# Optimization experiments

Hardware: AMD Instinct MI355X
Metric: run time of the kernel (lower is better)

The kernel has to match this reference:

```python
import jax, jax.numpy as jnp
import numpy as np
from jax import lax

H = 128

def lstm_layer(x, w_ih, w_hh, b):
    # x: [T,B,I]; w_ih: [4H,I]; w_hh: [4H,H]; b: [4H] (b_ih+b_hh combined)
    T, B, _ = x.shape
    Hs = w_hh.shape[1]
    xg = jnp.einsum('tbi,gi->tbg', x, w_ih) + b  # precompute input projections [T,B,4H]
    def step(carry, xg_t):
        h, c = carry
        g = xg_t + h @ w_hh.T
        i, f, gg, o = jnp.split(g, 4, axis=-1)  # PyTorch gate order: i,f,g,o
        c = jax.nn.sigmoid(f) * c + jax.nn.sigmoid(i) * jnp.tanh(gg)
        h = jax.nn.sigmoid(o) * jnp.tanh(c)
        return (h, c), h
    init = (jnp.zeros((B, Hs), x.dtype), jnp.zeros((B, Hs), x.dtype))
    (h_n, c_n), hs = lax.scan(step, init, xg)
    return hs, (h_n, c_n)

def setup_inputs() -> dict:
    key = jax.random.key(0)
    ks = jax.random.split(key, 12)
    V, T, B = 32000, 512, 64
    s = 1.0 / np.sqrt(H)
    u = lambda k, sh: jax.random.uniform(k, sh, jnp.float32, -s, s)
    return {
        'inputs': jax.random.randint(ks[0], (T, B), 0, V),
        'emb': jax.random.normal(ks[1], (V, H), jnp.float32),
        'w_ih0': u(ks[2], (2, 4 * H, H)),      # bidirectional layer 0 (fwd, bwd)
        'w_hh0': u(ks[3], (2, 4 * H, H)),
        'b0':    u(ks[4], (2, 4 * H)),
        'w_ih1': u(ks[5], (4 * H, 2 * H)),     # layer 1 consumes concat of both directions
        'w_hh1': u(ks[6], (4 * H, H)),
        'b1':    u(ks[7], (4 * H)),
        'w_ihr': u(ks[8], (6, 4 * H, H)),      # layers 2..7 (residual)
        'w_hhr': u(ks[9], (6, 4 * H, H)),
        'br':    u(ks[10], (6, 4 * H)),
    }

def reference(inputs, emb, w_ih0, w_hh0, b0, w_ih1, w_hh1, b1, w_ihr, w_hhr, br):
    x = emb[inputs]                                   # [T,B,H]
    # layer 0: bidirectional
    hf, _ = lstm_layer(x, w_ih0[0], w_hh0[0], b0[0])
    hb, _ = lstm_layer(x[::-1], w_ih0[1], w_hh0[1], b0[1])
    x = jnp.concatenate([hf, hb[::-1]], axis=-1)      # [T,B,2H]
    # layer 1: 2H -> H
    x, hidden = lstm_layer(x, w_ih1, w_hh1, b1)
    # layers 2..7 with residual adds
    for i in range(w_ihr.shape[0]):
        residual = x
        x, hidden = lstm_layer(x, w_ihr[i], w_hhr[i], br[i])
        x = x + residual
    h_n, c_n = hidden
    return x, h_n[None], c_n[None]
```

## Files before the change

kernel.cpp:

```cpp
#include <hip/hip_runtime.h>
#include <hip/hip_bf16.h>

#define TT 512
#define BB 64
#define HH 128
#define GG 512
#define TBH (TT*BB*HH)
#define TBG (TT*BB*GG)
#define BH (BB*HH)
#define CH 64
#define NCH (TT/CH)
#define CHGG (CH*BB*GG)
#define CHH (CH*BB*HH)

__device__ __forceinline__ float bflo(unsigned u) { return __uint_as_float(u << 16); }
__device__ __forceinline__ float bfhi(unsigned u) { return __uint_as_float(u & 0xffff0000u); }
__device__ __forceinline__ float ldf(const void* p, size_t i, int isbf) {
  return isbf ? __uint_as_float(((unsigned)((const unsigned short*)p)[i]) << 16)
              : ((const float*)p)[i];
}

template<int CTRL>
__device__ __forceinline__ float dpp_add(float v) {
  int r = __builtin_amdgcn_mov_dpp(__float_as_int(v), CTRL, 0xF, 0xF, true);
  return v + __int_as_float(r);
}

__device__ __forceinline__ float sigm(float x) {
  return __builtin_amdgcn_rcpf(1.f + __expf(-x));
}
__device__ __forceinline__ float tanh_f(float x) {
  return fmaf(2.f, __builtin_amdgcn_rcpf(1.f + __expf(-2.f * x)), -1.f);
}

__device__ __forceinline__ void ldw16(const void* W, size_t off, int isbf, float4* out) {
  if (isbf) {
    const uint4* wp = (const uint4*)W;
    uint4 v0 = wp[(off >> 3) + 0];
    uint4 v1 = wp[(off >> 3) + 1];
    out[0] = make_float4(bflo(v0.x), bfhi(v0.x), bflo(v0.y), bfhi(v0.y));
    out[1] = make_float4(bflo(v0.z), bfhi(v0.z), bflo(v0.w), bfhi(v0.w));
    out[2] = make_float4(bflo(v1.x), bfhi(v1.x), bflo(v1.y), bfhi(v1.y));
    out[3] = make_float4(bflo(v1.z), bfhi(v1.z), bflo(v1.w), bfhi(v1.w));
  } else {
    const float4* wp = (const float4*)W;
    out[0] = wp[(off >> 2) + 0]; out[1] = wp[(off >> 2) + 1];
    out[2] = wp[(off >> 2) + 2]; out[3] = wp[(off >> 2) + 3];
  }
}

__global__ __launch_bounds__(256) void k_detect(const unsigned* __restrict__ bits,
                                                unsigned* __restrict__ flag) {
  __shared__ int cnt;
  if (threadIdx.x == 0) cnt = 0;
  __syncthreads();
  int local = 0;
  for (int i = threadIdx.x; i < 1024; i += 256) {
    unsigned e = (bits[i] >> 7) & 0xff;
    if (e >= 118 && e <= 134) local++;
  }
  atomicAdd(&cnt, local);
  __syncthreads();
  if (threadIdx.x == 0) *flag = (cnt > 768) ? 1u : 0u;
}

__global__ __launch_bounds__(256) void k_embed(const int* __restrict__ idx,
                                               const void* __restrict__ emb,
                                               const unsigned* __restrict__ flag,
                                               float* __restrict__ x0) {
  int isbf = (int)*flag;
  int i = blockIdx.x * 256 + threadIdx.x;
  int h = i & (HH - 1);
  int tb = i >> 7;
  x0[i] = ldf(emb, (size_t)idx[tb] * HH + h, isbf);
}

__global__ __launch_bounds__(256) void k_proj(const float* __restrict__ A,
                                              const void* __restrict__ W, size_t w_off,
                                              const void* __restrict__ bias, size_t b_off,
                                              float* __restrict__ C, int K,
                                              const unsigned* __restrict__ flag) {
  int isbf = (int)*flag;
  __shared__ float As[16][68];
  __shared__ float Bs[16][68];
  int tid = threadIdx.x;
  int tx = tid & 15, ty = tid >> 4;
  int m_base = blockIdx.x * 64, n_base = blockIdx.y * 64;
  float acc[4][4] = {};
  int kk = tid & 15, rr = tid >> 4;
  for (int k0 = 0; k0 < K; k0 += 16) {
    #pragma unroll
    for (int r = 0; r < 4; r++) {
      As[kk][rr + 16*r] = A[(size_t)(m_base + rr + 16*r) * K + k0 + kk];
      Bs[kk][rr + 16*r] = ldf(W, w_off + (size_t)(n_base + rr + 16*r) * K + k0 + kk, isbf);
    }
    __syncthreads();
    #pragma unroll
    for (int k = 0; k < 16; k++) {
      float4 av = *(const float4*)(&As[k][ty*4]);
      float4 bv = *(const float4*)(&Bs[k][tx*4]);
      float a[4] = {av.x, av.y, av.z, av.w};
      float b[4] = {bv.x, bv.y, bv.z, bv.w};
      #pragma unroll
      for (int i = 0; i < 4; i++)
        #pragma unroll
        for (int j = 0; j < 4; j++)
          acc[i][j] += a[i] * b[j];
    }
    __syncthreads();
  }
  #pragma unroll
  for (int i = 0; i < 4; i++) {
    #pragma unroll
    for (int j = 0; j < 4; j++) {
      int n = n_base + tx*4 + j;
      C[(size_t)(m_base + ty*4 + i) * GG + n] = acc[i][j] + ldf(bias, b_off + n, isbf);
    }
  }
}

__global__ __launch_bounds__(512, 2) void k_recur(
    const float* __restrict__ xg, size_t xg_dstride,
    const void* __restrict__ whh, size_t w_off, size_t w_dstride,
    float* __restrict__ hout, int hout_stride, int hout_doff,
    const float* __restrict__ res,
    float* __restrict__ hfin, float* __restrict__ cfin,
    int bidir, const unsigned* __restrict__ flag) {
  int isbf = (int)*flag;
  int d = blockIdx.x >> 6;
  int b = blockIdx.x & 63;
  int dir = (bidir == 2 || (bidir == 1 && d)) ? -1 : 1;
  xg += (size_t)d * xg_dstride;
  size_t woff = w_off + (size_t)d * w_dstride;
  int hcol = hout_doff * d;

  int t0 = threadIdx.x;
  int j = t0 >> 2, q = t0 & 3;

  float w[4][32];
  size_t wbase = woff + (size_t)j * HH + q * 32;
  if (isbf) {
    const uint4* wp = (const uint4*)whh;
    #pragma unroll
    for (int g = 0; g < 4; g++) {
      size_t b8 = (wbase + (size_t)g * 128 * HH) >> 3;
      #pragma unroll
      for (int u = 0; u < 4; u++) {
        uint4 v = wp[b8 + ((u + q) & 3)];
        w[g][u*8+0] = bflo(v.x); w[g][u*8+1] = bfhi(v.x);
        w[g][u*8+2] = bflo(v.y); w[g][u*8+3] = bfhi(v.y);
        w[g][u*8+4] = bflo(v.z); w[g][u*8+5] = bfhi(v.z);
        w[g][u*8+6] = bflo(v.w); w[g][u*8+7] = bfhi(v.w);
      }
    }
  } else {
    const float4* wp = (const float4*)whh;
    #pragma unroll
    for (int g = 0; g < 4; g++) {
      size_t b4 = (wbase + (size_t)g * 128 * HH) >> 2;
      #pragma unroll
      for (int u = 0; u < 8; u++) {
        float4 v = wp[b4 + ((u + 2*q) & 7)];
        w[g][u*4+0] = v.x; w[g][u*4+1] = v.y; w[g][u*4+2] = v.z; w[g][u*4+3] = v.w;
      }
    }
  }

  __shared__ float h_lds[2][HH];
  if (t0 < HH) h_lds[0][t0] = 0.f;
  float c = 0.f;

  int tfirst = (dir > 0) ? 0 : (TT - 1);
  size_t rg0 = ((size_t)tfirst * BB + b) * GG;
  float xg_cur[4];
  #pragma unroll
  for (int g = 0; g < 4; g++) xg_cur[g] = xg[rg0 + g * HH + j];
  float res_cur = res ? res[((size_t)tfirst * BB + b) * HH + j] : 0.f;
  __syncthreads();

  const float* hc = h_lds[0];
  float* hn = h_lds[1];

  #pragma unroll 1
  for (int s = 0; s < TT; s++) {
    int t = (dir > 0) ? s : (TT - 1 - s);
    float xg_nxt[4] = {0.f, 0.f, 0.f, 0.f};
    float res_nxt = 0.f;
    if (s + 1 < TT) {
      int tn = (dir > 0) ? (s + 1) : (TT - 2 - s);
      size_t rg = ((size_t)tn * BB + b) * GG;
      #pragma unroll
      for (int g = 0; g < 4; g++) xg_nxt[g] = xg[rg + g * HH + j];
      if (res) res_nxt = res[((size_t)tn * BB + b) * HH + j];
    }
    float p0 = 0.f, p1 = 0.f, p2 = 0.f, p3 = 0.f;
    const float4* hq = (const float4*)(hc + (q << 5));
    #pragma unroll
    for (int u = 0; u < 8; u++) {
      float4 hv = hq[(u + 2*q) & 7];
      p0 = fmaf(w[0][u*4+0], hv.x, p0); p0 = fmaf(w[0][u*4+1], hv.y, p0);
      p0 = fmaf(w[0][u*4+2], hv.z, p0); p0 = fmaf(w[0][u*4+3], hv.w, p0);
      p1 = fmaf(w[1][u*4+0], hv.x, p1); p1 = fmaf(w[1][u*4+1], hv.y, p1);
      p1 = fmaf(w[1][u*4+2], hv.z, p1); p1 = fmaf(w[1][u*4+3], hv.w, p1);
      p2 = fmaf(w[2][u*4+0], hv.x, p2); p2 = fmaf(w[2][u*4+1], hv.y, p2);
      p2 = fmaf(w[2][u*4+2], hv.z, p2); p2 = fmaf(w[2][u*4+3], hv.w, p2);
      p3 = fmaf(w[3][u*4+0], hv.x, p3); p3 = fmaf(w[3][u*4+1], hv.y, p3);
      p3 = fmaf(w[3][u*4+2], hv.z, p3); p3 = fmaf(w[3][u*4+3], hv.w, p3);
    }
    p0 = dpp_add<0xB1>(p0); p0 = dpp_add<0x4E>(p0);
    p1 = dpp_add<0xB1>(p1); p1 = dpp_add<0x4E>(p1);
    p2 = dpp_add<0xB1>(p2); p2 = dpp_add<0x4E>(p2);
    p3 = dpp_add<0xB1>(p3); p3 = dpp_add<0x4E>(p3);

    float gi = p0 + xg_cur[0], gf = p1 + xg_cur[1];
    float gc = p2 + xg_cur[2], go = p3 + xg_cur[3];
    float si = sigm(gi), sf = sigm(gf), so = sigm(go);
    c = fmaf(sf, c, si * tanh_f(gc));
    float h = so * tanh_f(c);

    if (q == 0) {
      hn[j] = h;
      hout[((size_t)t * BB + b) * hout_stride + hcol + j] = h + res_cur;
      if (t == TT - 1) hfin[(size_t)(d * BB + b) * HH + j] = h;
    }
    #pragma unroll
    for (int g = 0; g < 4; g++) xg_cur[g] = xg_nxt[g];
    res_cur = res_nxt;
    __syncthreads();
    const float* tmp = hc; hc = hn; hn = (float*)tmp;
  }
  if (q == 0) cfin[(size_t)(d * BB + b) * HH + j] = c;
}

struct WaveDesc { int n; int r[8]; int k[8]; };

__device__ __forceinline__ void colgemm4(
    const float (*hch)[264], int K,
    const void* W, size_t wbase,
    const void* bias, size_t bias_off, int isbf,
    float* dstbase, int nn, int mh) {
  float acc[4][16];
  #pragma unroll
  for (int c = 0; c < 4; c++) {
    float bv = ldf(bias, bias_off + nn + 128*c, isbf);
    #pragma unroll
    for (int mi = 0; mi < 16; mi++) acc[c][mi] = bv;
  }
  #pragma unroll 1
  for (int kb = 0; kb < K; kb += 16) {
    float4 wcb[4][4];
    #pragma unroll
    for (int c = 0; c < 4; c++)
      ldw16(W, wbase + (size_t)(nn + 128*c) * K + kb, isbf, wcb[c]);
    #pragma unroll
    for (int mi = 0; mi < 16; mi++) {
      const float* hrow = &hch[mh*16 + mi][kb];
      float4 hv[4];
      hv[0] = *(const float4*)&hrow[0];
      hv[1] = *(const float4*)&hrow[4];
      hv[2] = *(const float4*)&hrow[8];
      hv[3] = *(const float4*)&hrow[12];
      #pragma unroll
      for (int c = 0; c < 4; c++) {
        #pragma unroll
        for (int u = 0; u < 4; u++) {
          acc[c][mi] = fmaf(wcb[c][u].x, hv[u].x, acc[c][mi]);
          acc[c][mi] = fmaf(wcb[c][u].y, hv[u].y, acc[c][mi]);
          acc[c][mi] = fmaf(wcb[c][u].z, hv[u].z, acc[c][mi]);
          acc[c][mi] = fmaf(wcb[c][u].w, hv[u].w, acc[c][mi]);
        }
      }
    }
  }
  #pragma unroll
  for (int mi = 0; mi < 16; mi++) {
    size_t mo = (size_t)(mh*16 + mi) * BB * GG;
    #pragma unroll
    for (int c = 0; c < 4; c++)
      dstbase[mo + nn + 128*c] = acc[c][mi];
  }
}

__global__ __launch_bounds__(512, 1) void k_wave(
    WaveDesc wd, float* __restrict__ xgf, float* __restrict__ xgb,
    const float* __restrict__ xcat, float* __restrict__ out7, float* __restrict__ scratch,
    const void* __restrict__ w_ih1, const void* __restrict__ w_hh1, const void* __restrict__ b1,
    const void* __restrict__ w_ihr, const void* __restrict__ w_hhr, const void* __restrict__ br,
    const unsigned* __restrict__ flag) {
  int isbf = (int)*flag;
  int slot = blockIdx.x >> 6;
  int b = blockIdx.x & 63;
  int r = wd.r[slot];
  int k = wd.k[slot];

  float* ringbase = xgb + 4 * (size_t)CHGG;
  float* hstate   = ringbase + 12 * (size_t)CHH;
  float* cstate   = hstate + 7 * (size_t)BH;

  auto xgslot = [&](int rr, int kk) -> float* {
    int s = (rr - 2) * 2 + (kk & 1);
    return (s < 8) ? (xgf + (size_t)s * CHGG) : (xgb + (size_t)(s - 8) * CHGG);
  };
  auto ringch = [&](int rr, int kk) -> float* {
    return ringbase + ((size_t)(rr - 1) * 2 + (kk & 1)) * CHH;
  };

  __shared__ float hchunk[CH][264];
  __shared__ float h_lds[2][HH];

  int t0 = threadIdx.x;
  int nn = t0 & 127;
  int mh = t0 >> 7;

  if (r == 1) {
    {
      int m = t0 >> 3, c0 = (t0 & 7) * 32;
      const float* src = xcat + ((size_t)(k * CH + m) * BB + b) * (2 * HH) + c0;
      #pragma unroll
      for (int u = 0; u < 8; u++)
        *(float4*)&hchunk[m][c0 + u * 4] = ((const float4*)src)[u];
    }
    __syncthreads();
    colgemm4(hchunk, 2 * HH, w_ih1, 0, b1, 0, isbf,
             scratch + (size_t)b * GG, nn, mh);
    __syncthreads();
  }

  const void* whh = (r == 1) ? w_hh1 : w_hhr;
  size_t woff = (r == 1) ? 0 : (size_t)(r - 2) * GG * HH;
  const float* xg = (r == 1) ? scratch : xgslot(r, k);
  const float* resb = (r >= 2) ? (ringch(r - 1, k) + (size_t)b * HH) : nullptr;
  float* houtb = (r == 7) ? (out7 + (size_t)k * CHH + (size_t)b * HH)
                          : (ringch(r, k) + (size_t)b * HH);
  float* hst = hstate + (size_t)(r - 1) * BH + (size_t)b * HH;
  float* cst = cstate + (size_t)(r - 1) * BH + (size_t)b * HH;

  int j = t0 >> 2, q = t0 & 3;

  float w[4][32];
  size_t wbase = woff + (size_t)j * HH + q * 32;
  if (isbf) {
    const uint4* wp = (const uint4*)whh;
    #pragma unroll
    for (int g = 0; g < 4; g++) {
      size_t b8 = (wbase + (size_t)g * 128 * HH) >> 3;
      #pragma unroll
      for (int u = 0; u < 4; u++) {
        uint4 v = wp[b8 + ((u + q) & 3)];
        w[g][u*8+0] = bflo(v.x); w[g][u*8+1] = bfhi(v.x);
        w[g][u*8+2] = bflo(v.y); w[g][u*8+3] = bfhi(v.y);
        w[g][u*8+4] = bflo(v.z); w[g][u*8+5] = bfhi(v.z);
        w[g][u*8+6] = bflo(v.w); w[g][u*8+7] = bfhi(v.w);
      }
    }
  } else {
    const float4* wp = (const float4*)whh;
    #pragma unroll
    for (int g = 0; g < 4; g++) {
      size_t b4 = (wbase + (size_t)g * 128 * HH) >> 2;
      #pragma unroll
      for (int u = 0; u < 8; u++) {
        float4 v = wp[b4 + ((u + 2*q) & 7)];
        w[g][u*4+0] = v.x; w[g][u*4+1] = v.y; w[g][u*4+2] = v.z; w[g][u*4+3] = v.w;
      }
    }
  }

  if (t0 < HH) h_lds[0][t0] = k ? hst[t0] : 0.f;
  float c = k ? cst[j] : 0.f;

  size_t rg0 = (size_t)b * GG;
  float xg_cur[4];
  #pragma unroll
  for (int g = 0; g < 4; g++) xg_cur[g] = xg[rg0 + g * HH + j];
  float res_cur = resb ? resb[j] : 0.f;
  __syncthreads();

  const float* hc = h_lds[0];
  float* hn = h_lds[1];

  #pragma unroll 1
  for (int s = 0; s < CH; s++) {
    float xg_nxt[4] = {0.f, 0.f, 0.f, 0.f};
    float res_nxt = 0.f;
    if (s + 1 < CH) {
      size_t rg = ((size_t)(s + 1) * BB + b) * GG;
      #pragma unroll
      for (int g = 0; g < 4; g++) xg_nxt[g] = xg[rg + g * HH + j];
      if (resb) res_nxt = resb[(size_t)(s + 1) * BB * HH + j];
    }
    float p0 = 0.f, p1 = 0.f, p2 = 0.f, p3 = 0.f;
    const float4* hq = (const float4*)(hc + (q << 5));
    #pragma unroll
    for (int u = 0; u < 8; u++) {
      float4 hv = hq[(u + 2*q) & 7];
      p0 = fmaf(w[0][u*4+0], hv.x, p0); p0 = fmaf(w[0][u*4+1], hv.y, p0);
      p0 = fmaf(w[0][u*4+2], hv.z, p0); p0 = fmaf(w[0][u*4+3], hv.w, p0);
      p1 = fmaf(w[1][u*4+0], hv.x, p1); p1 = fmaf(w[1][u*4+1], hv.y, p1);
      p1 = fmaf(w[1][u*4+2], hv.z, p1); p1 = fmaf(w[1][u*4+3], hv.w, p1);
      p2 = fmaf(w[2][u*4+0], hv.x, p2); p2 = fmaf(w[2][u*4+1], hv.y, p2);
      p2 = fmaf(w[2][u*4+2], hv.z, p2); p2 = fmaf(w[2][u*4+3], hv.w, p2);
      p3 = fmaf(w[3][u*4+0], hv.x, p3); p3 = fmaf(w[3][u*4+1], hv.y, p3);
      p3 = fmaf(w[3][u*4+2], hv.z, p3); p3 = fmaf(w[3][u*4+3], hv.w, p3);
    }
    p0 = dpp_add<0xB1>(p0); p0 = dpp_add<0x4E>(p0);
    p1 = dpp_add<0xB1>(p1); p1 = dpp_add<0x4E>(p1);
    p2 = dpp_add<0xB1>(p2); p2 = dpp_add<0x4E>(p2);
    p3 = dpp_add<0xB1>(p3); p3 = dpp_add<0x4E>(p3);

    float gi = p0 + xg_cur[0], gf = p1 + xg_cur[1];
    float gc = p2 + xg_cur[2], go = p3 + xg_cur[3];
    float si = sigm(gi), sf = sigm(gf), so = sigm(go);
    c = fmaf(sf, c, si * tanh_f(gc));
    float h = so * tanh_f(c);

    if (q == 0) {
      float hv = h + res_cur;
      hn[j] = h;
      hchunk[s][j] = hv;
      houtb[(size_t)s * BB * HH + j] = hv;
      if (s == CH - 1) hst[j] = h;
    }
    #pragma unroll
    for (int g = 0; g < 4; g++) xg_cur[g] = xg_nxt[g];
    res_cur = res_nxt;
    __syncthreads();
    const float* tmp = hc; hc = hn; hn = (float*)tmp;
  }
  if (q == 0) cst[j] = c;

  if (r < 7) {
    colgemm4(hchunk, HH, w_ihr, (size_t)(r - 1) * GG * HH,
             br, (size_t)(r - 1) * GG, isbf,
             xgslot(r + 1, k) + (size_t)b * GG, nn, mh);
  }
}

__global__ __launch_bounds__(256) void k_out(const float* __restrict__ x,
                                             const float* __restrict__ hfin,
                                             const float* __restrict__ cfin,
                                             void* __restrict__ out,
                                             const unsigned* __restrict__ flag) {
  int isbf = (int)*flag;
  int i = blockIdx.x * 256 + threadIdx.x;
  float v;
  if (i < TBH) v = x[i];
  else if (i < TBH + BH) v = hfin[i - TBH];
  else v = cfin[i - TBH - BH];
  if (isbf) ((__hip_bfloat16*)out)[i] = __float2bfloat16(v);
  else ((float*)out)[i] = v;
}

extern "C" void kernel_launch(void* const* d_in, const int* in_sizes, int n_in,
                              void* d_out, int out_size, void* d_ws, size_t ws_size,
                              hipStream_t stream) {
  const int* idx = (const int*)d_in[0];
  const void* emb   = d_in[1];
  const void* w_ih0 = d_in[2];
  const void* w_hh0 = d_in[3];
  const void* b0    = d_in[4];
  const void* w_ih1 = d_in[5];
  const void* w_hh1 = d_in[6];
  const void* b1    = d_in[7];
  const void* w_ihr = d_in[8];
  const void* w_hhr = d_in[9];
  const void* br    = d_in[10];

  float* ws   = (float*)d_ws;
  float* x0   = ws;
  float* xcat = ws + TBH;
  float* xg_f = ws + 3 * (size_t)TBH;
  float* hfin = ws + 3 * (size_t)TBH + TBG;
  float* cfin = hfin + 2 * BH;
  unsigned* flag = (unsigned*)(cfin + 2 * BH);
  float* xg_b = cfin + 2 * BH + 16384;
  int merged = ws_size >= (size_t)(3 * (size_t)TBH + 2 * (size_t)TBG + 4 * BH + 16384 + 64) * 4;

  k_detect<<<1, 256, 0, stream>>>((const unsigned*)emb, flag);
  k_embed<<<TBH / 256, 256, 0, stream>>>(idx, emb, flag, x0);

  dim3 pg(512, 8);
  if (merged) {
    k_proj<<<pg, 256, 0, stream>>>(x0, w_ih0, 0, b0, 0, xg_f, HH, flag);
    k_proj<<<pg, 256, 0, stream>>>(x0, w_ih0, (size_t)GG * HH, b0, GG, xg_b, HH, flag);
    k_recur<<<128, 512, 0, stream>>>(xg_f, (size_t)(xg_b - xg_f), w_hh0, 0, (size_t)GG * HH,
                                     xcat, 2 * HH, HH, nullptr, hfin, cfin, 1, flag);

    float* scratch = x0 + (size_t)TBH / 2;
    float* ringbase = xg_b + 4 * (size_t)CHGG;
    float* hstate  = ringbase + 12 * (size_t)CHH;
    float* cstate  = hstate + 7 * (size_t)BH;
    for (int wv = 0; wv <= 6 + (NCH - 1); wv++) {
      WaveDesc wd; wd.n = 0;
      for (int r = 1; r <= 7; r++) {
        int kk = wv - (r - 1);
        if (kk >= 0 && kk < NCH) { wd.r[wd.n] = r; wd.k[wd.n] = kk; wd.n++; }
      }
      if (wd.n)
        k_wave<<<wd.n * 64, 512, 0, stream>>>(wd, xg_f, xg_b, xcat, x0, scratch,
                                              w_ih1, w_hh1, b1, w_ihr, w_hhr, br, flag);
    }
    k_out<<<(TBH + 2 * BH) / 256, 256, 0, stream>>>(x0, hstate + 6 * BH, cstate + 6 * BH,
                                                    d_out, flag);
  } else {
    k_proj<<<pg, 256, 0, stream>>>(x0, w_ih0, 0, b0, 0, xg_f, HH, flag);
    k_recur<<<64, 512, 0, stream>>>(xg_f, 0, w_hh0, 0, 0,
                                    xcat, 2 * HH, 0, nullptr, hfin, cfin, 0, flag);
    k_proj<<<pg, 256, 0, stream>>>(x0, w_ih0, (size_t)GG * HH, b0, GG, xg_f, HH, flag);
    k_recur<<<64, 512, 0, stream>>>(xg_f, 0, w_hh0, (size_t)GG * HH, 0,
                                    xcat + HH, 2 * HH, 0, nullptr, hfin, cfin, 2, flag);
    float* xA = xcat;
    float* xB = xcat + TBH;
    k_proj<<<pg, 256, 0, stream>>>(xcat, w_ih1, 0, b1, 0, xg_f, 2 * HH, flag);
    k_recur<<<64, 512, 0, stream>>>(xg_f, 0, w_hh1, 0, 0, xA, HH, 0, nullptr, hfin, cfin, 0, flag);
    float* cur = xA;
    float* nxt = xB;
    for (int r = 0; r < 6; r++) {
      k_proj<<<pg, 256, 0, stream>>>(cur, w_ihr, (size_t)r * GG * HH, br, (size_t)r * GG, xg_f, HH, flag);
      k_recur<<<64, 512, 0, stream>>>(xg_f, 0, w_hhr, (size_t)r * GG * HH, 0,
                                      nxt, HH, 0, cur, hfin, cfin, 0, flag);
      float* t = cur; cur = nxt; nxt = t;
    }
    k_out<<<(TBH + 2 * BH) / 256, 256, 0, stream>>>(cur, hfin, cfin, d_out, flag);
  }
}
```

Before: 2.642 ms.

## Process two batch rows per block in wavefront LSTM kernel

Each k_wave block now runs the recurrence for two batch rows at once, so the grid shrinks from 64 to 32 blocks per wave slot. The register-held recurrent weights are reused across both rows, and the barrier and reduction costs of each time step are shared between them. In exchange each step does twice the serial FMA and transcendental work per thread with half as many blocks in flight. The chunk staging buffer in LDS is split into two 132-stride halves, one per row, and the input-projection GEMMs are run per row.

```diff
diff --git a/kernel.cpp b/kernel.cpp
--- a/kernel.cpp
+++ b/kernel.cpp
@@ -235,7 +235,7 @@
 struct WaveDesc { int n; int r[8]; int k[8]; };
 
 __device__ __forceinline__ void colgemm4(
-    const float (*hch)[264], int K,
+    const float* hch, int rstride, int K,
     const void* W, size_t wbase,
     const void* bias, size_t bias_off, int isbf,
     float* dstbase, int nn, int mh) {
@@ -254,7 +254,7 @@
       ldw16(W, wbase + (size_t)(nn + 128*c) * K + kb, isbf, wcb[c]);
     #pragma unroll
     for (int mi = 0; mi < 16; mi++) {
-      const float* hrow = &hch[mh*16 + mi][kb];
+      const float* hrow = hch + (size_t)(mh*16 + mi) * rstride + kb;
       float4 hv[4];
       hv[0] = *(const float4*)&hrow[0];
       hv[1] = *(const float4*)&hrow[4];
@@ -288,8 +288,9 @@
     const void* __restrict__ w_ihr, const void* __restrict__ w_hhr, const void* __restrict__ br,
     const unsigned* __restrict__ flag) {
   int isbf = (int)*flag;
-  int slot = blockIdx.x >> 6;
-  int b = blockIdx.x & 63;
+  int slot = blockIdx.x >> 5;
+  int bb = blockIdx.x & 31;
+  int bA = bb * 2, bB = bb * 2 + 1;
   int r = wd.r[slot];
   int k = wd.k[slot];
 
@@ -305,35 +306,44 @@
     return ringbase + ((size_t)(rr - 1) * 2 + (kk & 1)) * CHH;
   };
 
-  __shared__ float hchunk[CH][264];
-  __shared__ float h_lds[2][HH];
+  __shared__ float pool[CH * 264];
+  __shared__ float hldsA[2][HH];
+  __shared__ float hldsB[2][HH];
+  float* stg = pool;
+  float* pA  = pool;
+  float* pB  = pool + CH * 132;
 
   int t0 = threadIdx.x;
   int nn = t0 & 127;
   int mh = t0 >> 7;
 
   if (r == 1) {
-    {
-      int m = t0 >> 3, c0 = (t0 & 7) * 32;
-      const float* src = xcat + ((size_t)(k * CH + m) * BB + b) * (2 * HH) + c0;
-      #pragma unroll
-      for (int u = 0; u < 8; u++)
-        *(float4*)&hchunk[m][c0 + u * 4] = ((const float4*)src)[u];
-    }
-    __syncthreads();
-    colgemm4(hchunk, 2 * HH, w_ih1, 0, b1, 0, isbf,
-             scratch + (size_t)b * GG, nn, mh);
-    __syncthreads();
+    #pragma unroll 1
+    for (int pb = 0; pb < 2; pb++) {
+      int b = bA + pb;
+      {
+        int m = t0 >> 3, c0 = (t0 & 7) * 32;
+        const float* src = xcat + ((size_t)(k * CH + m) * BB + b) * (2 * HH) + c0;
+        #pragma unroll
+        for (int u = 0; u < 8; u++)
+          *(float4*)&stg[m * 264 + c0 + u * 4] = ((const float4*)src)[u];
+      }
+      __syncthreads();
+      colgemm4(stg, 264, 2 * HH, w_ih1, 0, b1, 0, isbf,
+               scratch + (size_t)b * GG, nn, mh);
+      __syncthreads();
+    }
   }
 
   const void* whh = (r == 1) ? w_hh1 : w_hhr;
   size_t woff = (r == 1) ? 0 : (size_t)(r - 2) * GG * HH;
   const float* xg = (r == 1) ? scratch : xgslot(r, k);
-  const float* resb = (r >= 2) ? (ringch(r - 1, k) + (size_t)b * HH) : nullptr;
-  float* houtb = (r == 7) ? (out7 + (size_t)k * CHH + (size_t)b * HH)
-                          : (ringch(r, k) + (size_t)b * HH);
-  float* hst = hstate + (size_t)(r - 1) * BH + (size_t)b * HH;
-  float* cst = cstate + (size_t)(r - 1) * BH + (size_t)b * HH;
+  const float* ringp = (r >= 2) ? ringch(r - 1, k) : nullptr;
+  float* houtbase = (r == 7) ? (out7 + (size_t)k * CHH) : ringch(r, k);
+  float* hstA = hstate + (size_t)(r - 1) * BH + (size_t)bA * HH;
+  float* hstB = hstate + (size_t)(r - 1) * BH + (size_t)bB * HH;
+  float* cstA = cstate + (size_t)(r - 1) * BH + (size_t)bA * HH;
+  float* cstB = cstate + (size_t)(r - 1) * BH + (size_t)bB * HH;
 
   int j = t0 >> 2, q = t0 & 3;
 
@@ -366,73 +376,114 @@
     }
   }
 
-  if (t0 < HH) h_lds[0][t0] = k ? hst[t0] : 0.f;
-  float c = k ? cst[j] : 0.f;
-
-  size_t rg0 = (size_t)b * GG;
-  float xg_cur[4];
+  if (t0 < HH) {
+    hldsA[0][t0] = k ? hstA[t0] : 0.f;
+    hldsB[0][t0] = k ? hstB[t0] : 0.f;
+  }
+  float cA = k ? cstA[j] : 0.f;
+  float cB = k ? cstB[j] : 0.f;
+
+  float xgA[4], xgB[4];
   #pragma unroll
-  for (int g = 0; g < 4; g++) xg_cur[g] = xg[rg0 + g * HH + j];
-  float res_cur = resb ? resb[j] : 0.f;
+  for (int g = 0; g < 4; g++) {
+    xgA[g] = xg[(size_t)bA * GG + g * HH + j];
+    xgB[g] = xg[(size_t)bB * GG + g * HH + j];
+  }
+  float resA = ringp ? ringp[(size_t)bA * HH + j] : 0.f;
+  float resB = ringp ? ringp[(size_t)bB * HH + j] : 0.f;
   __syncthreads();
 
-  const float* hc = h_lds[0];
-  float* hn = h_lds[1];
+  const float* hcA = hldsA[0];
+  const float* hcB = hldsB[0];
+  float* hnA = hldsA[1];
+  float* hnB = hldsB[1];
 
   #pragma unroll 1
   for (int s = 0; s < CH; s++) {
-    float xg_nxt[4] = {0.f, 0.f, 0.f, 0.f};
-    float res_nxt = 0.f;
+    float xgA_n[4] = {0.f,0.f,0.f,0.f}, xgB_n[4] = {0.f,0.f,0.f,0.f};
+    float resA_n = 0.f, resB_n = 0.f;
     if (s + 1 < CH) {
-      size_t rg = ((size_t)(s + 1) * BB + b) * GG;
-      #pragma unroll
-      for (int g = 0; g < 4; g++) xg_nxt[g] = xg[rg + g * HH + j];
-      if (resb) res_nxt = resb[(size_t)(s + 1) * BB * HH + j];
-    }
-    float p0 = 0.f, p1 = 0.f, p2 = 0.f, p3 = 0.f;
-    const float4* hq = (const float4*)(hc + (q << 5));
+      size_t rgA = ((size_t)(s + 1) * BB + bA) * GG;
+      #pragma unroll
+      for (int g = 0; g < 4; g++) {
+        xgA_n[g] = xg[rgA + g * HH + j];
+        xgB_n[g] = xg[rgA + GG + g * HH + j];
+      }
+      if (ringp) {
+        resA_n = ringp[((size_t)(s + 1) * BB + bA) * HH + j];
+        resB_n = ringp[((size_t)(s + 1) * BB + bB) * HH + j];
+      }
+    }
+    float pA0 = 0.f, pA1 = 0.f, pA2 = 0.f, pA3 = 0.f;
+    float pB0 = 0.f, pB1 = 0.f, pB2 = 0.f, pB3 = 0.f;
+    const float4* hqA = (const float4*)(hcA + (q << 5));
+    const float4* hqB = (const float4*)(hcB + (q << 5));
     #pragma unroll
     for (int u = 0; u < 8; u++) {
-      float4 hv = hq[(u + 2*q) & 7];
-      p0 = fmaf(w[0][u*4+0], hv.x, p0); p0 = fmaf(w[0][u*4+1], hv.y, p0);
-      p0 = fmaf(w[0][u*4+2], hv.z, p0); p0 = fmaf(w[0][u*4+3], hv.w, p0);
-      p1 = fmaf(w[1][u*4+0], hv.x, p1); p1 = fmaf(w[1][u*4+1], hv.y, p1);
-      p1 = fmaf(w[1][u*4+2], hv.z, p1); p1 = fmaf(w[1][u*4+3], hv.w, p1);
-      p2 = fmaf(w[2][u*4+0], hv.x, p2); p2 = fmaf(w[2][u*4+1], hv.y, p2);
-      p2 = fmaf(w[2][u*4+2], hv.z, p2); p2 = fmaf(w[2][u*4+3], hv.w, p2);
-      p3 = fmaf(w[3][u*4+0], hv.x, p3); p3 = fmaf(w[3][u*4+1], hv.y, p3);
-      p3 = fmaf(w[3][u*4+2], hv.z, p3); p3 = fmaf(w[3][u*4+3], hv.w, p3);
-    }
-    p0 = dpp_add<0xB1>(p0); p0 = dpp_add<0x4E>(p0);
-    p1 = dpp_add<0xB1>(p1); p1 = dpp_add<0x4E>(p1);
-    p2 = dpp_add<0xB1>(p2); p2 = dpp_add<0x4E>(p2);
-    p3 = dpp_add<0xB1>(p3); p3 = dpp_add<0x4E>(p3);
-
-    float gi = p0 + xg_cur[0], gf = p1 + xg_cur[1];
-    float gc = p2 + xg_cur[2], go = p3 + xg_cur[3];
-    float si = sigm(gi), sf = sigm(gf), so = sigm(go);
-    c = fmaf(sf, c, si * tanh_f(gc));
-    float h = so * tanh_f(c);
+      float4 a = hqA[(u + 2*q) & 7];
+      float4 e = hqB[(u + 2*q) & 7];
+      pA0 = fmaf(w[0][u*4+0], a.x, pA0); pA0 = fmaf(w[0][u*4+1], a.y, pA0);
+      pA0 = fmaf(w[0][u*4+2], a.z, pA0); pA0 = fmaf(w[0][u*4+3], a.w, pA0);
+      pA1 = fmaf(w[1][u*4+0], a.x, pA1); pA1 = fmaf(w[1][u*4+1], a.y, pA1);
+      pA1 = fmaf(w[1][u*4+2], a.z, pA1); pA1 = fmaf(w[1][u*4+3], a.w, pA1);
+      pA2 = fmaf(w[2][u*4+0], a.x, pA2); pA2 = fmaf(w[2][u*4+1], a.y, pA2);
+      pA2 = fmaf(w[2][u*4+2], a.z, pA2); pA2 = fmaf(w[2][u*4+3], a.w, pA2);
+      pA3 = fmaf(w[3][u*4+0], a.x, pA3); pA3 = fmaf(w[3][u*4+1], a.y, pA3);
+      pA3 = fmaf(w[3][u*4+2], a.z, pA3); pA3 = fmaf(w[3][u*4+3], a.w, pA3);
+      pB0 = fmaf(w[0][u*4+0], e.x, pB0); pB0 = fmaf(w[0][u*4+1], e.y, pB0);
+      pB0 = fmaf(w[0][u*4+2], e.z, pB0); pB0 = fmaf(w[0][u*4+3], e.w, pB0);
+      pB1 = fmaf(w[1][u*4+0], e.x, pB1); pB1 = fmaf(w[1][u*4+1], e.y, pB1);
+      pB1 = fmaf(w[1][u*4+2], e.z, pB1); pB1 = fmaf(w[1][u*4+3], e.w, pB1);
+      pB2 = fmaf(w[2][u*4+0], e.x, pB2); pB2 = fmaf(w[2][u*4+1], e.y, pB2);
+      pB2 = fmaf(w[2][u*4+2], e.z, pB2); pB2 = fmaf(w[2][u*4+3], e.w, pB2);
+      pB3 = fmaf(w[3][u*4+0], e.x, pB3); pB3 = fmaf(w[3][u*4+1], e.y, pB3);
+      pB3 = fmaf(w[3][u*4+2], e.z, pB3); pB3 = fmaf(w[3][u*4+3], e.w, pB3);
+    }
+    pA0 = dpp_add<0xB1>(pA0); pA0 = dpp_add<0x4E>(pA0);
+    pA1 = dpp_add<0xB1>(pA1); pA1 = dpp_add<0x4E>(pA1);
+    pA2 = dpp_add<0xB1>(pA2); pA2 = dpp_add<0x4E>(pA2);
+    pA3 = dpp_add<0xB1>(pA3); pA3 = dpp_add<0x4E>(pA3);
+    pB0 = dpp_add<0xB1>(pB0); pB0 = dpp_add<0x4E>(pB0);
+    pB1 = dpp_add<0xB1>(pB1); pB1 = dpp_add<0x4E>(pB1);
+    pB2 = dpp_add<0xB1>(pB2); pB2 = dpp_add<0x4E>(pB2);
+    pB3 = dpp_add<0xB1>(pB3); pB3 = dpp_add<0x4E>(pB3);
+
+    float giA = pA0 + xgA[0], gfA = pA1 + xgA[1];
+    float gcA = pA2 + xgA[2], goA = pA3 + xgA[3];
+    float siA = sigm(giA), sfA = sigm(gfA), soA = sigm(goA);
+    cA = fmaf(sfA, cA, siA * tanh_f(gcA));
+    float hA = soA * tanh_f(cA);
+
+    float giB = pB0 + xgB[0], gfB = pB1 + xgB[1];
+    float gcB = pB2 + xgB[2], goB = pB3 + xgB[3];
+    float siB = sigm(giB), sfB = sigm(gfB), soB = sigm(goB);
+    cB = fmaf(sfB, cB, siB * tanh_f(gcB));
+    float hB = soB * tanh_f(cB);
 
     if (q == 0) {
-      float hv = h + res_cur;
-      hn[j] = h;
-      hchunk[s][j] = hv;
-      houtb[(size_t)s * BB * HH + j] = hv;
-      if (s == CH - 1) hst[j] = h;
-    }
-    #pragma unroll
-    for (int g = 0; g < 4; g++) xg_cur[g] = xg_nxt[g];
-    res_cur = res_nxt;
+      float hvA = hA + resA, hvB = hB + resB;
+      hnA[j] = hA; hnB[j] = hB;
+      pA[s * 132 + j] = hvA;
+      pB[s * 132 + j] = hvB;
+      houtbase[((size_t)s * BB + bA) * HH + j] = hvA;
+      houtbase[((size_t)s * BB + bB) * HH + j] = hvB;
+      if (s == CH - 1) { hstA[j] = hA; hstB[j] = hB; }
+    }
+    #pragma unroll
+    for (int g = 0; g < 4; g++) { xgA[g] = xgA_n[g]; xgB[g] = xgB_n[g]; }
+    resA = resA_n; resB = resB_n;
     __syncthreads();
-    const float* tmp = hc; hc = hn; hn = (float*)tmp;
-  }
-  if (q == 0) cst[j] = c;
+    const float* t1 = hcA; hcA = hnA; hnA = (float*)t1;
+    const float* t2 = hcB; hcB = hnB; hnB = (float*)t2;
+  }
+  if (q == 0) { cstA[j] = cA; cstB[j] = cB; }
 
   if (r < 7) {
-    colgemm4(hchunk, HH, w_ihr, (size_t)(r - 1) * GG * HH,
-             br, (size_t)(r - 1) * GG, isbf,
-             xgslot(r + 1, k) + (size_t)b * GG, nn, mh);
+    size_t wb = (size_t)(r - 1) * GG * HH;
+    size_t bo = (size_t)(r - 1) * GG;
+    float* dslot = xgslot(r + 1, k);
+    colgemm4(pA, 132, HH, w_ihr, wb, br, bo, isbf, dslot + (size_t)bA * GG, nn, mh);
+    colgemm4(pB, 132, HH, w_ihr, wb, br, bo, isbf, dslot + (size_t)bB * GG, nn, mh);
   }
 }
 
@@ -497,7 +548,7 @@
         if (kk >= 0 && kk < NCH) { wd.r[wd.n] = r; wd.k[wd.n] = kk; wd.n++; }
       }
       if (wd.n)
-        k_wave<<<wd.n * 64, 512, 0, stream>>>(wd, xg_f, xg_b, xcat, x0, scratch,
+        k_wave<<<wd.n * 32, 512, 0, stream>>>(wd, xg_f, xg_b, xcat, x0, scratch,
                                               w_ih1, w_hh1, b1, w_ihr, w_hhr, br, flag);
     }
     k_out<<<(TBH + 2 * BH) / 256, 256, 0, stream>>>(x0, hstate + 6 * BH, cstate + 6 * BH,
```

New measurement: 3.975 ms. +50.5%, slower.
